# Optimization experiments

Measured on AMD Instinct MI355X. Metric: run time of the kernel, lower is better.

Reference implementation:

```python
import jax, jax.numpy as jnp
import numpy as np

D_MODEL = 2048
NUM_HEADS = 32
HEAD_DIM = D_MODEL // NUM_HEADS  # 64
ROPE_BASE = 10000.0


def _rope_cos_sin(seq_len, head_dim, dtype):
    inv_freq = 1.0 / (ROPE_BASE ** (jnp.arange(0, head_dim, 2, dtype=jnp.float32) / head_dim))
    freqs = jnp.arange(seq_len, dtype=jnp.float32)[:, None] * inv_freq[None, :]  # (S, Dh/2)
    emb = jnp.concatenate([freqs, freqs], axis=-1)  # (S, Dh)
    return emb.astype(dtype), jnp.cos(emb).astype(dtype), jnp.sin(emb).astype(dtype)


def _rotate_half(x):
    x1, x2 = jnp.split(x, 2, axis=-1)
    return jnp.concatenate([-x2, x1], axis=-1)


def setup_inputs() -> dict:
    key = jax.random.key(0)
    k1, k2, k3, k4 = jax.random.split(key, 4)
    B, S, D = 1, 2048, D_MODEL
    x = jax.random.normal(k1, (B, S, D), dtype=jnp.float32)
    Wqkv = jax.random.normal(k2, (3 * D, D), dtype=jnp.float32) * 0.02
    Wo = jax.random.normal(k3, (D, D), dtype=jnp.float32) * 0.02
    gate = jax.random.normal(k4, (D,), dtype=jnp.float32) * 0.1
    return {"x": x, "Wqkv": Wqkv, "Wo": Wo, "gate": gate}


def reference(x, Wqkv, Wo, gate):
    B, S, D = x.shape
    H, Dh = NUM_HEADS, HEAD_DIM
    residual = x

    # fused QKV projection (torch Linear: y = x @ W.T)
    qkv = jnp.einsum('bsd,ed->bse', x, Wqkv).reshape(B, S, 3, H, Dh)
    q, k, v = qkv[:, :, 0], qkv[:, :, 1], qkv[:, :, 2]  # each (B, S, H, Dh)

    # RoPE
    _, cos, sin = _rope_cos_sin(S, Dh, x.dtype)
    cos = cos[None, :, None, :]  # (1, S, 1, Dh)
    sin = sin[None, :, None, :]
    q = q * cos + _rotate_half(q) * sin
    k = k * cos + _rotate_half(k) * sin

    # causal SDPA
    scale = 1.0 / np.sqrt(Dh)
    scores = jnp.einsum('bqhd,bkhd->bhqk', q, k) * scale  # (B, H, S, S)
    causal = jnp.tril(jnp.ones((S, S), dtype=bool))
    scores = jnp.where(causal[None, None], scores, jnp.finfo(scores.dtype).min)
    probs = jax.nn.softmax(scores, axis=-1)
    attn = jnp.einsum('bhqk,bkhd->bqhd', probs, v).reshape(B, S, D)

    out = jnp.einsum('bsd,ed->bse', attn, Wo)
    # HeoGate: learned per-channel gated residual (assumption; see notes)
    return residual + gate * out
```

## Files before the change

### kernel.cpp

```cpp
#include <hip/hip_runtime.h>
#include <hip/hip_bf16.h>
#include <cstdint>
#include <cstddef>

typedef __hip_bfloat16 bf16;
typedef short short8 __attribute__((ext_vector_type(8)));
typedef float f32x4 __attribute__((ext_vector_type(4)));

#define S_LEN 2048
#define DMODEL 2048
#define NQKV 6144
#define NHEADS 32
#define HDIM 64

__device__ __forceinline__ void async_copy16(const bf16* g, bf16* l) {
  __builtin_amdgcn_global_load_lds(
      (const __attribute__((address_space(1))) void*)g,
      (__attribute__((address_space(3))) void*)l, 16, 0, 0);
}

__device__ __forceinline__ f32x4 mfma_bf16(short8 a, short8 b, f32x4 c) {
  return __builtin_amdgcn_mfma_f32_16x16x32_bf16(a, b, c, 0, 0, 0);
}

__global__ __launch_bounds__(256) void cvt3_kernel(const float* __restrict__ sx,
                                                   bf16* __restrict__ dx,
                                                   const float* __restrict__ sw,
                                                   bf16* __restrict__ dw,
                                                   const float* __restrict__ so,
                                                   bf16* __restrict__ dov) {
  int i = blockIdx.x * 256 + threadIdx.x;
  const float* s;
  bf16* d;
  if (i < 1048576) {
    s = sx; d = dx;
  } else if (i < 4194304) {
    s = sw; d = dw; i -= 1048576;
  } else {
    s = so; d = dov; i -= 4194304;
  }
  const float4 v = ((const float4*)s)[i];
  union { bf16 h[4]; ushort4 u; } tmp;
  tmp.h[0] = __float2bfloat16(v.x);
  tmp.h[1] = __float2bfloat16(v.y);
  tmp.h[2] = __float2bfloat16(v.z);
  tmp.h[3] = __float2bfloat16(v.w);
  ((ushort4*)d)[i] = tmp.u;
}

__global__ __launch_bounds__(256) void gemm_qkv(const bf16* __restrict__ A,
                                                const bf16* __restrict__ W,
                                                bf16* __restrict__ q_ws,
                                                bf16* __restrict__ k_ws,
                                                bf16* __restrict__ v_ws) {
  constexpr int K = DMODEL;
  __shared__ bf16 As[128 * 32];
  __shared__ bf16 Ws[128 * 32];
  const int tid = threadIdx.x;
  const int wave = tid >> 6, lane = tid & 63;
  const int wm = wave >> 1, wn = wave & 1;
  const int m0 = blockIdx.y * 128, n0 = blockIdx.x * 128;
  const int sr = wave * 16 + (lane >> 2);
  const int sc = (lane & 3) * 8;
  const int fr = lane & 15, fq = lane >> 4;

  const f32x4 zero = {0.f, 0.f, 0.f, 0.f};
  f32x4 acc[4][4];
  for (int i = 0; i < 4; ++i)
    for (int j = 0; j < 4; ++j) acc[i][j] = zero;

  for (int kt = 0; kt < K; kt += 32) {
    __syncthreads();
    for (int i2 = 0; i2 < 2; ++i2) {
      async_copy16(A + (size_t)(m0 + i2 * 64 + sr) * K + kt + sc,
                   &As[(i2 * 64 + wave * 16) * 32]);
      async_copy16(W + (size_t)(n0 + i2 * 64 + sr) * K + kt + sc,
                   &Ws[(i2 * 64 + wave * 16) * 32]);
    }
    __syncthreads();
    short8 a[4], b[4];
    for (int i = 0; i < 4; ++i)
      a[i] = *(const short8*)&As[(wm * 64 + i * 16 + fr) * 32 + fq * 8];
    for (int j = 0; j < 4; ++j)
      b[j] = *(const short8*)&Ws[(wn * 64 + j * 16 + fr) * 32 + fq * 8];
    for (int i = 0; i < 4; ++i)
      for (int j = 0; j < 4; ++j)
        acc[i][j] = mfma_bf16(a[i], b[j], acc[i][j]);
  }

  const int colb = n0 + wn * 64;
  const int sect = colb >> 11;
  const int h = (colb & 2047) >> 6;
  const int col = fr, rq = fq * 4;

  if (sect < 2) {
    bf16* dst = ((sect == 0) ? q_ws : k_ws) + (size_t)h * S_LEN * HDIM;
    for (int jl = 0; jl < 2; ++jl) {
      const int dh = jl * 16 + col;
      const float freq = powf(10000.0f, -(float)dh * (1.0f / 32.0f));
      for (int i = 0; i < 4; ++i) {
        const int base_row = m0 + wm * 64 + i * 16 + rq;
        for (int r = 0; r < 4; ++r) {
          const int srow = base_row + r;
          float sn, cs;
          sincosf((float)srow * freq, &sn, &cs);
          const float xl = acc[i][jl][r], xh = acc[i][jl + 2][r];
          dst[(size_t)srow * HDIM + dh]      = __float2bfloat16(xl * cs - xh * sn);
          dst[(size_t)srow * HDIM + dh + 32] = __float2bfloat16(xh * cs + xl * sn);
        }
      }
    }
  } else {
    bf16* dst = v_ws + (size_t)h * S_LEN * HDIM;
    for (int j = 0; j < 4; ++j) {
      const int dh = j * 16 + col;
      for (int i = 0; i < 4; ++i) {
        const int base_row = m0 + wm * 64 + i * 16 + rq;
        for (int r = 0; r < 4; ++r)
          dst[(size_t)(base_row + r) * HDIM + dh] = __float2bfloat16(acc[i][j][r]);
      }
    }
  }
}

__global__ __launch_bounds__(256) void transpose_v(const bf16* __restrict__ v,
                                                   bf16* __restrict__ vt) {
  __shared__ bf16 t[64 * 66];
  const int h = blockIdx.y, s0 = blockIdx.x * 64;
  const int tid = threadIdx.x;
  const bf16* src = v + (size_t)h * S_LEN * HDIM;
  bf16* dst = vt + (size_t)h * HDIM * S_LEN;
  for (int rep = 0; rep < 16; ++rep) {
    const int idx = rep * 256 + tid;
    const int sl = idx >> 6, dh = idx & 63;
    t[sl * 66 + dh] = src[(size_t)(s0 + sl) * HDIM + dh];
  }
  __syncthreads();
  for (int rep = 0; rep < 16; ++rep) {
    const int idx = rep * 256 + tid;
    const int dh = idx >> 6, sl = idx & 63;
    dst[(size_t)dh * S_LEN + s0 + sl] = t[sl * 66 + dh];
  }
}

__global__ __launch_bounds__(256) void attn_kernel(const bf16* __restrict__ q_ws,
                                                   const bf16* __restrict__ k_ws,
                                                   const bf16* __restrict__ vt_ws,
                                                   bf16* __restrict__ attn_out) {
  const int bid = blockIdx.x;
  const int qt = 31 - (bid >> 5);
  const int h = bid & 31;

  const int tid = threadIdx.x, wave = tid >> 6, lane = tid & 63;
  const int col = lane & 15, fq = lane >> 4;
  const int q_glob = qt * 64 + wave * 16 + col;

  __shared__ bf16 Ks[2][64 * 64];
  __shared__ bf16 Vs[2][64 * 64];
  __shared__ bf16 Pl[4][16 * 72];
  bf16* pl = Pl[wave];

  const bf16* qh = q_ws + (size_t)h * S_LEN * HDIM;
  const bf16* kh = k_ws + (size_t)h * S_LEN * HDIM;
  const bf16* vh = vt_ws + (size_t)h * HDIM * S_LEN;

  const int srow = lane >> 3;
  const int slot = lane & 7;
  const int schunk = slot ^ srow;

  auto stage = [&](int kt, int buf) {
    const int k0 = kt * 64;
#pragma unroll
    for (int j = 0; j < 2; ++j) {
      const int r8 = (wave * 2 + j) * 8;
      async_copy16(kh + (size_t)(k0 + r8 + srow) * HDIM + schunk * 8,
                   &Ks[buf][r8 * 64]);
      async_copy16(vh + (size_t)(r8 + srow) * S_LEN + k0 + schunk * 8,
                   &Vs[buf][r8 * 64]);
    }
  };

  short8 qf[2];
#pragma unroll
  for (int ks = 0; ks < 2; ++ks)
    qf[ks] = *(const short8*)&qh[(size_t)q_glob * HDIM + ks * 32 + fq * 8];

  const f32x4 zero = {0.f, 0.f, 0.f, 0.f};
  f32x4 o_acc[4] = {zero, zero, zero, zero};
  float m_i = -1e30f, l_i = 0.f;

  stage(0, 0);

  for (int kt = 0; kt <= qt; ++kt) {
    const int buf = kt & 1;
    const int k0 = kt * 64;
    __syncthreads();
    if (kt < qt) stage(kt + 1, buf ^ 1);

    short8 kf[8];
#pragma unroll
    for (int n = 0; n < 4; ++n) {
      const int row = n * 16 + col;
#pragma unroll
      for (int ks = 0; ks < 2; ++ks)
        kf[n * 2 + ks] =
            *(const short8*)&Ks[buf][row * 64 + (((ks * 4 + fq) ^ (row & 7)) * 8)];
    }
    f32x4 s_acc[4] = {zero, zero, zero, zero};
#pragma unroll
    for (int n = 0; n < 4; ++n)
#pragma unroll
      for (int ks = 0; ks < 2; ++ks)
        s_acc[n] = mfma_bf16(kf[n * 2 + ks], qf[ks], s_acc[n]);

    short8 vf[8];
#pragma unroll
    for (int n = 0; n < 4; ++n) {
      const int row = n * 16 + col;
#pragma unroll
      for (int ks = 0; ks < 2; ++ks)
        vf[n * 2 + ks] =
            *(const short8*)&Vs[buf][row * 64 + (((ks * 4 + fq) ^ (row & 7)) * 8)];
    }

    if (kt == qt) {
#pragma unroll
      for (int n = 0; n < 4; ++n)
#pragma unroll
        for (int r = 0; r < 4; ++r)
          if (k0 + n * 16 + fq * 4 + r > q_glob) s_acc[n][r] = -1e30f;
    }

    float vmax = -1e30f;
#pragma unroll
    for (int n = 0; n < 4; ++n)
#pragma unroll
      for (int r = 0; r < 4; ++r) vmax = fmaxf(vmax, s_acc[n][r]);
    vmax = fmaxf(vmax, __shfl_xor(vmax, 16, 64));
    vmax = fmaxf(vmax, __shfl_xor(vmax, 32, 64));
    const float mnew = fmaxf(m_i, vmax);
    const float alpha = __expf((m_i - mnew) * 0.125f);
    m_i = mnew;

    float rs = 0.f;
#pragma unroll
    for (int n = 0; n < 4; ++n)
#pragma unroll
      for (int r = 0; r < 4; ++r) {
        const float p = __expf((s_acc[n][r] - mnew) * 0.125f);
        s_acc[n][r] = p;
        rs += p;
      }
    rs += __shfl_xor(rs, 16, 64);
    rs += __shfl_xor(rs, 32, 64);
    l_i = l_i * alpha + rs;

#pragma unroll
    for (int n = 0; n < 4; ++n)
#pragma unroll
      for (int r = 0; r < 4; ++r) o_acc[n][r] *= alpha;

#pragma unroll
    for (int n = 0; n < 4; ++n) {
      union { bf16 hx[4]; uint2 u; } pk;
#pragma unroll
      for (int r = 0; r < 4; ++r) pk.hx[r] = __float2bfloat16(s_acc[n][r]);
      *(uint2*)&pl[col * 72 + n * 16 + fq * 4] = pk.u;
    }
    short8 pa[2];
#pragma unroll
    for (int ks = 0; ks < 2; ++ks)
      pa[ks] = *(const short8*)&pl[col * 72 + ks * 32 + fq * 8];

#pragma unroll
    for (int n = 0; n < 4; ++n)
#pragma unroll
      for (int ks = 0; ks < 2; ++ks)
        o_acc[n] = mfma_bf16(vf[n * 2 + ks], pa[ks], o_acc[n]);
  }

  const float inv = 1.0f / l_i;
#pragma unroll
  for (int n = 0; n < 4; ++n) {
#pragma unroll
    for (int r = 0; r < 4; ++r) o_acc[n][r] *= inv;
    union { bf16 hx[4]; uint2 u; } ok;
#pragma unroll
    for (int r = 0; r < 4; ++r) ok.hx[r] = __float2bfloat16(o_acc[n][r]);
    *(uint2*)&attn_out[(size_t)q_glob * DMODEL + h * HDIM + n * 16 + fq * 4] = ok.u;
  }
}

__global__ __launch_bounds__(256) void gemm_out(const bf16* __restrict__ A,
                                                const bf16* __restrict__ W,
                                                const float* __restrict__ xres,
                                                const float* __restrict__ gate,
                                                float* __restrict__ out) {
  constexpr int K = DMODEL;
  __shared__ bf16 As[128 * 32];
  __shared__ bf16 Ws[128 * 32];
  const int tid = threadIdx.x;
  const int wave = tid >> 6, lane = tid & 63;
  const int wm = wave >> 1, wn = wave & 1;
  const int m0 = blockIdx.y * 128, n0 = blockIdx.x * 128;
  const int sr = wave * 16 + (lane >> 2);
  const int sc = (lane & 3) * 8;
  const int fr = lane & 15, fq = lane >> 4;

  const f32x4 zero = {0.f, 0.f, 0.f, 0.f};
  f32x4 acc[4][4];
  for (int i = 0; i < 4; ++i)
    for (int j = 0; j < 4; ++j) acc[i][j] = zero;

  for (int kt = 0; kt < K; kt += 32) {
    __syncthreads();
    for (int i2 = 0; i2 < 2; ++i2) {
      async_copy16(A + (size_t)(m0 + i2 * 64 + sr) * K + kt + sc,
                   &As[(i2 * 64 + wave * 16) * 32]);
      async_copy16(W + (size_t)(n0 + i2 * 64 + sr) * K + kt + sc,
                   &Ws[(i2 * 64 + wave * 16) * 32]);
    }
    __syncthreads();
    short8 a[4], b[4];
    for (int i = 0; i < 4; ++i)
      a[i] = *(const short8*)&As[(wm * 64 + i * 16 + fr) * 32 + fq * 8];
    for (int j = 0; j < 4; ++j)
      b[j] = *(const short8*)&Ws[(wn * 64 + j * 16 + fr) * 32 + fq * 8];
    for (int i = 0; i < 4; ++i)
      for (int j = 0; j < 4; ++j)
        acc[i][j] = mfma_bf16(a[i], b[j], acc[i][j]);
  }

  const int col = fr, rq = fq * 4;
  for (int j = 0; j < 4; ++j) {
    const int cc = n0 + wn * 64 + j * 16 + col;
    const float g = gate[cc];
    for (int i = 0; i < 4; ++i) {
      const int base_row = m0 + wm * 64 + i * 16 + rq;
      for (int r = 0; r < 4; ++r) {
        const size_t idx = (size_t)(base_row + r) * DMODEL + cc;
        out[idx] = xres[idx] + g * acc[i][j][r];
      }
    }
  }
}

extern "C" void kernel_launch(void* const* d_in, const int* in_sizes, int n_in,
                              void* d_out, int out_size, void* d_ws, size_t ws_size,
                              hipStream_t stream) {
  const float* x    = (const float*)d_in[0];
  const float* Wqkv = (const float*)d_in[1];
  const float* Wo   = (const float*)d_in[2];
  const float* gate = (const float*)d_in[3];
  float* out = (float*)d_out;

  char* ws = (char*)d_ws;
  const size_t MB = 1024 * 1024;
  bf16* xb      = (bf16*)(ws);
  bf16* wqkvb   = (bf16*)(ws + 8 * MB);
  bf16* wob     = (bf16*)(ws + 32 * MB);
  bf16* q_ws    = (bf16*)(ws + 40 * MB);
  bf16* k_ws    = (bf16*)(ws + 48 * MB);
  bf16* v_ws    = (bf16*)(ws + 56 * MB);
  bf16* vt_ws   = (bf16*)(ws + 8 * MB);
  bf16* attn_ws = (bf16*)(ws);

  cvt3_kernel<<<dim3(20480), 256, 0, stream>>>(x, xb, Wqkv, wqkvb, Wo, wob);

  gemm_qkv<<<dim3(NQKV / 128, DMODEL / 128), 256, 0, stream>>>(xb, wqkvb, q_ws, k_ws, v_ws);
  transpose_v<<<dim3(S_LEN / 64, NHEADS), 256, 0, stream>>>(v_ws, vt_ws);
  attn_kernel<<<dim3(1024), 256, 0, stream>>>(q_ws, k_ws, vt_ws, attn_ws);
  gemm_out<<<dim3(DMODEL / 128, DMODEL / 128), 256, 0, stream>>>(attn_ws, wob, x, gate, out);
}
```

Before: 299.5 us.

## Swizzle GEMM LDS tiles, fuse V transpose into QKV epilogue, stage RoPE stores

Applies an XOR swizzle to the LDS tile layout in both GEMMs to reduce bank conflicts on fragment reads. The QKV epilogue now writes V directly in transposed layout, which removes the separate transpose kernel and its extra round trip through memory. Q/K RoPE results are staged through shared memory so global stores become 16-byte row writes. RoPE frequencies come from exp2f and fast __sincosf, which may lose some accuracy at large angles.

```diff
diff --git a/kernel.cpp b/kernel.cpp
--- a/kernel.cpp
+++ b/kernel.cpp
@@ -12,6 +12,7 @@
 #define NQKV 6144
 #define NHEADS 32
 #define HDIM 64
+#define ROPE_L2 0.4152410118609203f
 
 __device__ __forceinline__ void async_copy16(const bf16* g, bf16* l) {
   __builtin_amdgcn_global_load_lds(
@@ -54,15 +55,16 @@
                                                 bf16* __restrict__ k_ws,
                                                 bf16* __restrict__ v_ws) {
   constexpr int K = DMODEL;
-  __shared__ bf16 As[128 * 32];
-  __shared__ bf16 Ws[128 * 32];
+  __shared__ bf16 smem[8192];
   const int tid = threadIdx.x;
   const int wave = tid >> 6, lane = tid & 63;
   const int wm = wave >> 1, wn = wave & 1;
   const int m0 = blockIdx.y * 128, n0 = blockIdx.x * 128;
   const int sr = wave * 16 + (lane >> 2);
-  const int sc = (lane & 3) * 8;
+  const int swc = (((lane & 3) ^ ((lane >> 3) & 3)) * 8);
   const int fr = lane & 15, fq = lane >> 4;
+  const int xw = (fr >> 1) & 3;
+  const int rdc = ((fq ^ xw) * 8);
 
   const f32x4 zero = {0.f, 0.f, 0.f, 0.f};
   f32x4 acc[4][4];
@@ -72,17 +74,17 @@
   for (int kt = 0; kt < K; kt += 32) {
     __syncthreads();
     for (int i2 = 0; i2 < 2; ++i2) {
-      async_copy16(A + (size_t)(m0 + i2 * 64 + sr) * K + kt + sc,
-                   &As[(i2 * 64 + wave * 16) * 32]);
-      async_copy16(W + (size_t)(n0 + i2 * 64 + sr) * K + kt + sc,
-                   &Ws[(i2 * 64 + wave * 16) * 32]);
+      async_copy16(A + (size_t)(m0 + i2 * 64 + sr) * K + kt + swc,
+                   &smem[(i2 * 64 + wave * 16) * 32]);
+      async_copy16(W + (size_t)(n0 + i2 * 64 + sr) * K + kt + swc,
+                   &smem[4096 + (i2 * 64 + wave * 16) * 32]);
     }
     __syncthreads();
     short8 a[4], b[4];
     for (int i = 0; i < 4; ++i)
-      a[i] = *(const short8*)&As[(wm * 64 + i * 16 + fr) * 32 + fq * 8];
+      a[i] = *(const short8*)&smem[(wm * 64 + i * 16 + fr) * 32 + rdc];
     for (int j = 0; j < 4; ++j)
-      b[j] = *(const short8*)&Ws[(wn * 64 + j * 16 + fr) * 32 + fq * 8];
+      b[j] = *(const short8*)&smem[4096 + (wn * 64 + j * 16 + fr) * 32 + rdc];
     for (int i = 0; i < 4; ++i)
       for (int j = 0; j < 4; ++j)
         acc[i][j] = mfma_bf16(a[i], b[j], acc[i][j]);
@@ -95,51 +97,45 @@
 
   if (sect < 2) {
     bf16* dst = ((sect == 0) ? q_ws : k_ws) + (size_t)h * S_LEN * HDIM;
-    for (int jl = 0; jl < 2; ++jl) {
-      const int dh = jl * 16 + col;
-      const float freq = powf(10000.0f, -(float)dh * (1.0f / 32.0f));
-      for (int i = 0; i < 4; ++i) {
-        const int base_row = m0 + wm * 64 + i * 16 + rq;
+    bf16* rep = smem + wave * 1152;
+    const float f0 = exp2f(-(float)col * ROPE_L2);
+    const float f1 = exp2f(-(float)(16 + col) * ROPE_L2);
+    __syncthreads();
+    for (int i = 0; i < 4; ++i) {
+      const int base_s = m0 + wm * 64 + i * 16;
+#pragma unroll
+      for (int jl = 0; jl < 2; ++jl) {
+        const int dh = jl * 16 + col;
+        const float fr_ = (jl == 0) ? f0 : f1;
+#pragma unroll
         for (int r = 0; r < 4; ++r) {
-          const int srow = base_row + r;
+          const int srow = base_s + rq + r;
           float sn, cs;
-          sincosf((float)srow * freq, &sn, &cs);
+          __sincosf((float)srow * fr_, &sn, &cs);
           const float xl = acc[i][jl][r], xh = acc[i][jl + 2][r];
-          dst[(size_t)srow * HDIM + dh]      = __float2bfloat16(xl * cs - xh * sn);
-          dst[(size_t)srow * HDIM + dh + 32] = __float2bfloat16(xh * cs + xl * sn);
+          rep[(rq + r) * 72 + dh]      = __float2bfloat16(xl * cs - xh * sn);
+          rep[(rq + r) * 72 + dh + 32] = __float2bfloat16(xh * cs + xl * sn);
         }
       }
+#pragma unroll
+      for (int p = 0; p < 2; ++p) {
+        const int rr = p * 8 + (lane >> 3), ch = lane & 7;
+        const uint4 vv = *(const uint4*)&rep[rr * 72 + ch * 8];
+        *(uint4*)&dst[(size_t)(base_s + rr) * HDIM + ch * 8] = vv;
+      }
     }
   } else {
-    bf16* dst = v_ws + (size_t)h * S_LEN * HDIM;
+    bf16* dst = v_ws + (size_t)h * HDIM * S_LEN;
     for (int j = 0; j < 4; ++j) {
       const int dh = j * 16 + col;
       for (int i = 0; i < 4; ++i) {
-        const int base_row = m0 + wm * 64 + i * 16 + rq;
-        for (int r = 0; r < 4; ++r)
-          dst[(size_t)(base_row + r) * HDIM + dh] = __float2bfloat16(acc[i][j][r]);
-      }
-    }
-  }
-}
-
-__global__ __launch_bounds__(256) void transpose_v(const bf16* __restrict__ v,
-                                                   bf16* __restrict__ vt) {
-  __shared__ bf16 t[64 * 66];
-  const int h = blockIdx.y, s0 = blockIdx.x * 64;
-  const int tid = threadIdx.x;
-  const bf16* src = v + (size_t)h * S_LEN * HDIM;
-  bf16* dst = vt + (size_t)h * HDIM * S_LEN;
-  for (int rep = 0; rep < 16; ++rep) {
-    const int idx = rep * 256 + tid;
-    const int sl = idx >> 6, dh = idx & 63;
-    t[sl * 66 + dh] = src[(size_t)(s0 + sl) * HDIM + dh];
-  }
-  __syncthreads();
-  for (int rep = 0; rep < 16; ++rep) {
-    const int idx = rep * 256 + tid;
-    const int dh = idx >> 6, sl = idx & 63;
-    dst[(size_t)dh * S_LEN + s0 + sl] = t[sl * 66 + dh];
+        const int s0 = m0 + wm * 64 + i * 16 + rq;
+        union { bf16 hx[4]; uint2 u; } vk;
+#pragma unroll
+        for (int r = 0; r < 4; ++r) vk.hx[r] = __float2bfloat16(acc[i][j][r]);
+        *(uint2*)&dst[(size_t)dh * S_LEN + s0] = vk.u;
+      }
+    }
   }
 }
 
@@ -304,8 +300,9 @@
   const int wm = wave >> 1, wn = wave & 1;
   const int m0 = blockIdx.y * 128, n0 = blockIdx.x * 128;
   const int sr = wave * 16 + (lane >> 2);
-  const int sc = (lane & 3) * 8;
+  const int swc = (((lane & 3) ^ ((lane >> 3) & 3)) * 8);
   const int fr = lane & 15, fq = lane >> 4;
+  const int rdc = ((fq ^ ((fr >> 1) & 3)) * 8);
 
   const f32x4 zero = {0.f, 0.f, 0.f, 0.f};
   f32x4 acc[4][4];
@@ -315,17 +312,17 @@
   for (int kt = 0; kt < K; kt += 32) {
     __syncthreads();
     for (int i2 = 0; i2 < 2; ++i2) {
-      async_copy16(A + (size_t)(m0 + i2 * 64 + sr) * K + kt + sc,
+      async_copy16(A + (size_t)(m0 + i2 * 64 + sr) * K + kt + swc,
                    &As[(i2 * 64 + wave * 16) * 32]);
-      async_copy16(W + (size_t)(n0 + i2 * 64 + sr) * K + kt + sc,
+      async_copy16(W + (size_t)(n0 + i2 * 64 + sr) * K + kt + swc,
                    &Ws[(i2 * 64 + wave * 16) * 32]);
     }
     __syncthreads();
     short8 a[4], b[4];
     for (int i = 0; i < 4; ++i)
-      a[i] = *(const short8*)&As[(wm * 64 + i * 16 + fr) * 32 + fq * 8];
+      a[i] = *(const short8*)&As[(wm * 64 + i * 16 + fr) * 32 + rdc];
     for (int j = 0; j < 4; ++j)
-      b[j] = *(const short8*)&Ws[(wn * 64 + j * 16 + fr) * 32 + fq * 8];
+      b[j] = *(const short8*)&Ws[(wn * 64 + j * 16 + fr) * 32 + rdc];
     for (int i = 0; i < 4; ++i)
       for (int j = 0; j < 4; ++j)
         acc[i][j] = mfma_bf16(a[i], b[j], acc[i][j]);
@@ -362,13 +359,11 @@
   bf16* q_ws    = (bf16*)(ws + 40 * MB);
   bf16* k_ws    = (bf16*)(ws + 48 * MB);
   bf16* v_ws    = (bf16*)(ws + 56 * MB);
-  bf16* vt_ws   = (bf16*)(ws + 8 * MB);
   bf16* attn_ws = (bf16*)(ws);
 
   cvt3_kernel<<<dim3(20480), 256, 0, stream>>>(x, xb, Wqkv, wqkvb, Wo, wob);
 
   gemm_qkv<<<dim3(NQKV / 128, DMODEL / 128), 256, 0, stream>>>(xb, wqkvb, q_ws, k_ws, v_ws);
-  transpose_v<<<dim3(S_LEN / 64, NHEADS), 256, 0, stream>>>(v_ws, vt_ws);
-  attn_kernel<<<dim3(1024), 256, 0, stream>>>(q_ws, k_ws, vt_ws, attn_ws);
+  attn_kernel<<<dim3(1024), 256, 0, stream>>>(q_ws, k_ws, v_ws, attn_ws);
   gemm_out<<<dim3(DMODEL / 128, DMODEL / 128), 256, 0, stream>>>(attn_ws, wob, x, gate, out);
 }
```

Measured after the change: 259.3 us. 1.16x faster.
